# Kernel optimization log

Measured on AMD Instinct MI355X. Metric: run time of the kernel, lower is better.

Reference implementation:

```python
import jax, jax.numpy as jnp
import numpy as np

TEMP = 0.07
BASE_TEMP = 0.07
LOSS_WEIGHT = 0.5
BN_EPS = 1e-5


def _embed(x, w1, b1, gamma, beta, w2, b2):
    # 1x1 conv C->C  (x: [N,C,H,W], w1: [C_out,C_in])
    h = jnp.einsum('nchw,oc->nohw', x, w1) + b1[None, :, None, None]
    # BatchNorm2d in training mode: batch stats over (N,H,W), biased variance
    mean = h.mean(axis=(0, 2, 3), keepdims=True)
    var = h.var(axis=(0, 2, 3), keepdims=True)
    h = (h - mean) * jax.lax.rsqrt(var + BN_EPS)
    h = h * gamma[None, :, None, None] + beta[None, :, None, None]
    h = jax.nn.relu(h)
    h = jnp.einsum('nchw,oc->nohw', h, w2) + b2[None, :, None, None]
    # F.normalize(p=2, dim=1) with eps=1e-12
    nrm = jnp.sqrt(jnp.sum(h * h, axis=1, keepdims=True))
    return h / jnp.maximum(nrm, 1e-12)


def _contrastive(feats_, labels_):
    # feats_: [T, n_view, C]; labels_: [T]
    T, n_view, C = feats_.shape
    mask_small = (labels_[:, None] == labels_[None, :]).astype(feats_.dtype)  # [T,T]
    # torch.cat(torch.unbind(feats_, dim=1), dim=0): view-major ordering
    cf = feats_.transpose(1, 0, 2).reshape(T * n_view, C)
    logits = (cf @ cf.T) / TEMP                                   # [M,M], M=T*n_view
    logits = logits - jax.lax.stop_gradient(jnp.max(logits, axis=1, keepdims=True))
    mask = jnp.tile(mask_small, (n_view, n_view))                  # repeat(anchor_count, contrast_count)
    neg_mask = 1.0 - mask                                          # computed BEFORE diagonal removal
    M = T * n_view
    logits_mask = 1.0 - jnp.eye(M, dtype=feats_.dtype)
    mask = mask * logits_mask
    exp_logits = jnp.exp(logits)
    neg_logits = jnp.sum(exp_logits * neg_mask, axis=1, keepdims=True)
    log_prob = logits - jnp.log(exp_logits + neg_logits)
    mean_log_prob_pos = jnp.sum(mask * log_prob, axis=1) / (jnp.sum(mask, axis=1) + 1e-6)
    loss = -(TEMP / BASE_TEMP) * mean_log_prob_pos
    return jnp.mean(loss)


def setup_inputs() -> dict:
    N, C_in, H, W = 8, 512, 128, 128
    feat_dim, num_classes = 256, 19
    max_views, max_samples, ignore_label = 100, 1024, -1
    rng = np.random.RandomState(0)

    preds_S = rng.randn(N, C_in, H, W).astype(np.float32)
    # gt label map already at (H,W) => nearest interpolation is identity
    gt = rng.randint(0, num_classes, (N, H * W))
    logits_S = rng.randn(N, num_classes, H * W).astype(np.float32)
    predict = logits_S.argmax(axis=1)  # [N, H*W]

    # ---- replicate _hard_anchor_sampling on host (fixed seed) ----
    classes, total = [], 0
    for i in range(N):
        cl = [int(c) for c in np.unique(gt[i])
              if c != ignore_label and (gt[i] == c).sum() > max_views]
        classes.append(cl)
        total += len(cl)
    n_view = min(max_samples // total, max_views)

    b_idx, p_idx, y_cls = [], [], []
    for i in range(N):
        for c in classes[i]:
            hard = np.where((predict[i] == c) & (gt[i] != c))[0]
            easy = np.where((predict[i] == c) & (gt[i] == c))[0]
            nh, ne = len(hard), len(easy)
            if nh >= n_view / 2 and ne >= n_view / 2:
                kh = n_view // 2; ke = n_view - kh
            elif nh >= n_view / 2:
                ke = ne; kh = n_view - ke
            else:
                kh = nh; ke = n_view - kh
            hs = hard[rng.permutation(nh)[:kh]]
            es = easy[rng.permutation(ne)[:ke]]
            b_idx.append(i)
            p_idx.append(np.concatenate([hs, es]))
            y_cls.append(c)

    batch_idx = jnp.asarray(np.array(b_idx), dtype=jnp.int32)          # [T]
    pix_idx = jnp.asarray(np.stack(p_idx), dtype=jnp.int32)            # [T, n_view]
    y_cls = jnp.asarray(np.array(y_cls), dtype=jnp.int32)              # [T]

    def p(shape, scale, k):
        r = np.random.RandomState(k)
        return jnp.asarray((r.randn(*shape) * scale).astype(np.float32))

    return {
        'preds_S': jnp.asarray(preds_S),
        'w1': p((C_in, C_in), 0.02, 1),
        'b1': jnp.zeros((C_in,), jnp.float32),
        'gamma': jnp.ones((C_in,), jnp.float32),
        'beta': jnp.zeros((C_in,), jnp.float32),
        'w2': p((feat_dim, C_in), 0.02, 2),
        'b2': jnp.zeros((feat_dim,), jnp.float32),
        'batch_idx': batch_idx,
        'pix_idx': pix_idx,
        'y_cls': y_cls,
    }


def reference(preds_S, w1, b1, gamma, beta, w2, b2, batch_idx, pix_idx, y_cls):
    f = _embed(preds_S, w1, b1, gamma, beta, w2, b2)        # [N, C, H, W]
    N, C, H, W = f.shape
    feats = f.transpose(0, 2, 3, 1).reshape(N, H * W, C)     # [N, HW, C]
    X_ = feats[batch_idx[:, None], pix_idx]                   # [T, n_view, C]
    labels_ = y_cls.astype(f.dtype)
    return LOSS_WEIGHT * _contrastive(X_, labels_)
```

## Files before the change

kernel.cpp:

```cpp
#include <hip/hip_runtime.h>
#include <hip/hip_bf16.h>

#define C_IN   512
#define C_OUT  256
#define HW     16384
#define NIMG   8
#define PTOT   (NIMG * HW)
#define MP     1024
#define TEMP_INV (1.0f / 0.07f)
#define BN_EPS   1e-5f
#define SPB    4
#define OGRP   8
#define IGRP   8
#define BK     64

typedef float  f32x4  __attribute__((ext_vector_type(4)));
typedef short  short8 __attribute__((ext_vector_type(8)));
typedef short  short4v __attribute__((ext_vector_type(4)));

#define WS_S1   0
#define WS_G    (WS_S1 + C_IN)
#define WS_W1P  (WS_G + C_IN * C_IN)
#define WS_B1P  (WS_W1P + C_IN * C_IN)
#define WS_CF   (WS_B1P + C_IN)
#define WS_XB_F (WS_CF + MP * C_OUT)
#define WS_NEED_FAST ((size_t)WS_XB_F * 4 + (size_t)PTOT * C_IN * 2)

__global__ __launch_bounds__(256)
void kprep(const float* __restrict__ x, __hip_bfloat16* __restrict__ xb,
           float* __restrict__ s1) {
    int plane = blockIdx.x;
    int c = plane & (C_IN - 1);
    const float4* p = (const float4*)(x + (size_t)plane * HW);
    short4v* q = (short4v*)(xb + (size_t)plane * HW);
    float acc = 0.f;
    for (int i = threadIdx.x; i < HW / 4; i += 256) {
        float4 v = p[i];
        acc += v.x + v.y + v.z + v.w;
        union { short4v s; __hip_bfloat162 h[2]; } u;
        u.h[0] = __float22bfloat162_rn(make_float2(v.x, v.y));
        u.h[1] = __float22bfloat162_rn(make_float2(v.z, v.w));
        q[i] = u.s;
    }
    for (int off = 32; off; off >>= 1) acc += __shfl_down(acc, off, 64);
    __shared__ float red[4];
    int lane = threadIdx.x & 63, wv = threadIdx.x >> 6;
    if (lane == 0) red[wv] = acc;
    __syncthreads();
    if (threadIdx.x == 0)
        atomicAdd(&s1[c], red[0] + red[1] + red[2] + red[3]);
}

__global__ __launch_bounds__(256)
void ksum(const float* __restrict__ x, float* __restrict__ s1) {
    int plane = blockIdx.x;
    int c = plane & (C_IN - 1);
    const float4* p = (const float4*)(x + (size_t)plane * HW);
    float acc = 0.f;
    for (int i = threadIdx.x; i < HW / 4; i += 256) {
        float4 v = p[i];
        acc += v.x + v.y + v.z + v.w;
    }
    for (int off = 32; off; off >>= 1) acc += __shfl_down(acc, off, 64);
    __shared__ float red[4];
    int lane = threadIdx.x & 63, wv = threadIdx.x >> 6;
    if (lane == 0) red[wv] = acc;
    __syncthreads();
    if (threadIdx.x == 0)
        atomicAdd(&s1[c], red[0] + red[1] + red[2] + red[3]);
}

__device__ const int TILE_I[10] = {0,0,0,0,1,1,1,2,2,3};
__device__ const int TILE_J[10] = {0,1,2,3,1,2,3,2,3,3};

__global__ __launch_bounds__(256, 4)
void kgram_bf16(const __hip_bfloat16* __restrict__ xb, float* __restrict__ G) {
    __shared__ __hip_bfloat16 Abuf[128 * BK];
    __shared__ __hip_bfloat16 Bbuf[128 * BK];
    int tile  = blockIdx.x;
    int chunk = blockIdx.y;
    int n   = chunk >> 4;
    int hw0 = (chunk & 15) * 1024;
    int wave = threadIdx.x >> 6;
    int lane = threadIdx.x & 63;
    int wi = wave >> 1, wj = wave & 1;
    int IT = TILE_I[tile] * 128;
    int JT = TILE_J[tile] * 128;

    const __hip_bfloat16* gA = xb + ((size_t)n * C_IN + IT) * HW + hw0;
    const __hip_bfloat16* gB = xb + ((size_t)n * C_IN + JT) * HW + hw0;

    int rrel = lane >> 3;
    int slot = lane & 7;

    f32x4 acc[4][4];
#pragma unroll
    for (int i = 0; i < 4; ++i)
#pragma unroll
        for (int j = 0; j < 4; ++j) acc[i][j] = {0.f, 0.f, 0.f, 0.f};

    int m  = lane & 15;
    int kq = lane >> 4;

#pragma unroll 1
    for (int s = 0; s < 16; ++s) {
        int kk = s * BK;
#pragma unroll
        for (int i_ = 0; i_ < 4; ++i_) {
            int row = wave * 32 + i_ * 8 + rrel;
            int g   = slot ^ (row & 7);
            __builtin_amdgcn_global_load_lds(
                (const __attribute__((address_space(1))) void*)
                    (gA + (size_t)row * HW + kk + g * 8),
                (__attribute__((address_space(3))) void*)
                    (&Abuf[(wave * 32 + i_ * 8) * BK]),
                16, 0, 0);
            __builtin_amdgcn_global_load_lds(
                (const __attribute__((address_space(1))) void*)
                    (gB + (size_t)row * HW + kk + g * 8),
                (__attribute__((address_space(3))) void*)
                    (&Bbuf[(wave * 32 + i_ * 8) * BK]),
                16, 0, 0);
        }
        __syncthreads();
#pragma unroll
        for (int h = 0; h < 2; ++h) {
            short8 af[4], bf[4];
#pragma unroll
            for (int t = 0; t < 4; ++t) {
                int ra = wi * 64 + t * 16 + m;
                int qa = (h * 4 + kq) ^ (ra & 7);
                af[t] = *(const short8*)&Abuf[ra * BK + qa * 8];
                int rb = wj * 64 + t * 16 + m;
                int qb = (h * 4 + kq) ^ (rb & 7);
                bf[t] = *(const short8*)&Bbuf[rb * BK + qb * 8];
            }
#pragma unroll
            for (int i_ = 0; i_ < 4; ++i_)
#pragma unroll
                for (int j_ = 0; j_ < 4; ++j_)
                    acc[i_][j_] = __builtin_amdgcn_mfma_f32_16x16x32_bf16(
                        af[i_], bf[j_], acc[i_][j_], 0, 0, 0);
        }
        __syncthreads();
    }

    int r0 = (lane >> 4) * 4;
    int cc = lane & 15;
#pragma unroll
    for (int i = 0; i < 4; ++i)
#pragma unroll
        for (int j = 0; j < 4; ++j)
#pragma unroll
            for (int r = 0; r < 4; ++r)
                atomicAdd(&G[(size_t)(IT + wi * 64 + i * 16 + r0 + r) * C_IN
                             + (JT + wj * 64 + j * 16 + cc)],
                          acc[i][j][r]);
}

__global__ __launch_bounds__(256)
void kmirror(float* __restrict__ G) {
    int i = blockIdx.x;
    for (int j = threadIdx.x; j < C_IN; j += 256) {
        if ((i >> 7) > (j >> 7))
            G[(size_t)i * C_IN + j] = G[(size_t)j * C_IN + i];
    }
}

__device__ inline short8 load_frag_f32(const float* p) {
    float4 a = *(const float4*)p;
    float4 b = *(const float4*)(p + 4);
    union { short8 s; __hip_bfloat162 h[4]; } u;
    u.h[0] = __float22bfloat162_rn(make_float2(a.x, a.y));
    u.h[1] = __float22bfloat162_rn(make_float2(a.z, a.w));
    u.h[2] = __float22bfloat162_rn(make_float2(b.x, b.y));
    u.h[3] = __float22bfloat162_rn(make_float2(b.z, b.w));
    return u.s;
}

__global__ __launch_bounds__(256)
void kgram_f32(const float* __restrict__ x, float* __restrict__ G) {
    int bz  = blockIdx.z;
    int n   = bz >> 2;
    int hw0 = (bz & 3) * 4096;
    int wave = threadIdx.x >> 6;
    int lane = threadIdx.x & 63;
    int wi = wave >> 1, wj = wave & 1;
    int I0 = blockIdx.x * 128 + wi * 64;
    int J0 = blockIdx.y * 128 + wj * 64;
    int m    = lane & 15;
    int koff = (lane >> 4) * 8;

    const float* baseA[4];
    const float* baseB[4];
#pragma unroll
    for (int t = 0; t < 4; ++t) {
        baseA[t] = x + ((size_t)n * C_IN + (I0 + t * 16 + m)) * HW + hw0 + koff;
        baseB[t] = x + ((size_t)n * C_IN + (J0 + t * 16 + m)) * HW + hw0 + koff;
    }

    f32x4 acc[4][4];
#pragma unroll
    for (int i = 0; i < 4; ++i)
#pragma unroll
        for (int j = 0; j < 4; ++j) acc[i][j] = {0.f, 0.f, 0.f, 0.f};

    for (int kk = 0; kk < 4096; kk += 32) {
        short8 afr[4], bfr[4];
#pragma unroll
        for (int t = 0; t < 4; ++t) {
            afr[t] = load_frag_f32(baseA[t] + kk);
            bfr[t] = load_frag_f32(baseB[t] + kk);
        }
#pragma unroll
        for (int i = 0; i < 4; ++i)
#pragma unroll
            for (int j = 0; j < 4; ++j)
                acc[i][j] = __builtin_amdgcn_mfma_f32_16x16x32_bf16(
                    afr[i], bfr[j], acc[i][j], 0, 0, 0);
    }

    int r0 = (lane >> 4) * 4;
    int cc = lane & 15;
#pragma unroll
    for (int i = 0; i < 4; ++i)
#pragma unroll
        for (int j = 0; j < 4; ++j)
#pragma unroll
            for (int r = 0; r < 4; ++r)
                atomicAdd(&G[(size_t)(I0 + i * 16 + r0 + r) * C_IN + (J0 + j * 16 + cc)],
                          acc[i][j][r]);
}

__global__ __launch_bounds__(256)
void kstats(const float* __restrict__ w1, const float* __restrict__ b1,
            const float* __restrict__ gamma, const float* __restrict__ beta,
            const float* __restrict__ s1, const float* __restrict__ G,
            float* __restrict__ w1p, float* __restrict__ b1p) {
    int o0 = blockIdx.x * OGRP;
    int tid = threadIdx.x;
    __shared__ float wr[OGRP][C_IN];
    __shared__ float redd[4][OGRP];
    __shared__ float redq[4][OGRP];
    __shared__ float alpha_s[OGRP];

    for (int idx = tid; idx < OGRP * C_IN; idx += 256) {
        int og = idx >> 9, c = idx & (C_IN - 1);
        wr[og][c] = w1[(size_t)(o0 + og) * C_IN + c];
    }
    __syncthreads();

    float dot1[OGRP], quad[OGRP];
#pragma unroll
    for (int og = 0; og < OGRP; ++og) { dot1[og] = 0.f; quad[og] = 0.f; }

    for (int c = tid; c < C_IN; c += 256) {
        const float* gr = G + (size_t)c * C_IN;
        float s1c = s1[c];
        float inner[OGRP];
#pragma unroll
        for (int og = 0; og < OGRP; ++og) inner[og] = 0.f;
        for (int d = 0; d < C_IN; d += 4) {
            float4 gv = *(const float4*)(gr + d);
#pragma unroll
            for (int og = 0; og < OGRP; ++og) {
                float4 wv = *(const float4*)(&wr[og][d]);
                inner[og] += gv.x * wv.x + gv.y * wv.y + gv.z * wv.z + gv.w * wv.w;
            }
        }
#pragma unroll
        for (int og = 0; og < OGRP; ++og) {
            float wc = wr[og][c];
            quad[og] += inner[og] * wc;
            dot1[og] += s1c * wc;
        }
    }
#pragma unroll
    for (int og = 0; og < OGRP; ++og) {
        for (int off = 32; off; off >>= 1) {
            dot1[og] += __shfl_down(dot1[og], off, 64);
            quad[og] += __shfl_down(quad[og], off, 64);
        }
    }
    int lane = tid & 63, wv = tid >> 6;
    if (lane == 0) {
#pragma unroll
        for (int og = 0; og < OGRP; ++og) { redd[wv][og] = dot1[og]; redq[wv][og] = quad[og]; }
    }
    __syncthreads();
    if (tid < OGRP) {
        int og = tid;
        float d1 = redd[0][og] + redd[1][og] + redd[2][og] + redd[3][og];
        float q  = redq[0][og] + redq[1][og] + redq[2][og] + redq[3][og];
        float b  = b1[o0 + og];
        float mean = d1 / (float)PTOT + b;
        float eh2  = (q + 2.f * b * d1) / (float)PTOT + b * b;
        float var  = eh2 - mean * mean;
        float al   = gamma[o0 + og] * rsqrtf(var + BN_EPS);
        alpha_s[og] = al;
        b1p[o0 + og] = beta[o0 + og] + al * (b - mean);
    }
    __syncthreads();
    for (int idx = tid; idx < OGRP * C_IN; idx += 256) {
        int og = idx >> 9, c = idx & (C_IN - 1);
        w1p[(size_t)(o0 + og) * C_IN + c] = alpha_s[og] * wr[og][c];
    }
}

__global__ __launch_bounds__(256)
void kfeat(const float* __restrict__ x, const float* __restrict__ w1p,
           const float* __restrict__ b1p, const float* __restrict__ w2,
           const float* __restrict__ b2, const int* __restrict__ batch_idx,
           const int* __restrict__ pix_idx, float* __restrict__ cf,
           int M, int T, int n_view) {
    __shared__ float xcol[SPB][C_IN];
    __shared__ float h1[SPB][C_IN];
    __shared__ float fl[SPB][C_OUT];
    int tid = threadIdx.x;
    int m0 = blockIdx.x * SPB;

    for (int idx = tid; idx < SPB * C_IN; idx += 256) {
        int s = idx >> 9, c = idx & (C_IN - 1);
        int mm = m0 + s;
        float v = 0.f;
        if (mm < M) {
            int t = mm % T, vv = mm / T;
            int n = batch_idx[t];
            int pix = pix_idx[t * n_view + vv];
            v = x[((size_t)n * C_IN + c) * HW + pix];
        }
        xcol[s][c] = v;
    }
    __syncthreads();

    for (int o = tid; o < C_IN; o += 256) {
        float acc[SPB];
        float bb = b1p[o];
#pragma unroll
        for (int s = 0; s < SPB; ++s) acc[s] = bb;
        const float* wrp = w1p + (size_t)o * C_IN;
        for (int c = 0; c < C_IN; c += 4) {
            float4 w = *(const float4*)(wrp + c);
#pragma unroll
            for (int s = 0; s < SPB; ++s) {
                float4 xv = *(const float4*)(&xcol[s][c]);
                acc[s] += w.x * xv.x + w.y * xv.y + w.z * xv.z + w.w * xv.w;
            }
        }
#pragma unroll
        for (int s = 0; s < SPB; ++s) h1[s][o] = fmaxf(acc[s], 0.f);
    }
    __syncthreads();

    {
        int j = tid;
        float acc[SPB];
        float bb = b2[j];
#pragma unroll
        for (int s = 0; s < SPB; ++s) acc[s] = bb;
        const float* wrp = w2 + (size_t)j * C_IN;
        for (int o = 0; o < C_IN; o += 4) {
            float4 w = *(const float4*)(wrp + o);
#pragma unroll
            for (int s = 0; s < SPB; ++s) {
                float4 hv = *(const float4*)(&h1[s][o]);
                acc[s] += w.x * hv.x + w.y * hv.y + w.z * hv.z + w.w * hv.w;
            }
        }
#pragma unroll
        for (int s = 0; s < SPB; ++s) fl[s][j] = acc[s];
    }
    __syncthreads();

    int wv = tid >> 6, lane = tid & 63;
    {
        float sq = 0.f;
#pragma unroll
        for (int k = 0; k < 4; ++k) { float v = fl[wv][lane + 64 * k]; sq += v * v; }
        for (int off = 32; off; off >>= 1) sq += __shfl_down(sq, off, 64);
        float nrm = __shfl(sq, 0, 64);
        float rinv = 1.f / fmaxf(sqrtf(nrm), 1e-12f);
        int mm = m0 + wv;
        if (mm < M) {
#pragma unroll
            for (int k = 0; k < 4; ++k)
                cf[(size_t)mm * C_OUT + lane + 64 * k] = fl[wv][lane + 64 * k] * rinv;
        }
    }
}

__global__ __launch_bounds__(256)
void kloss(const float* __restrict__ cf, const int* __restrict__ y_cls,
           float* __restrict__ out, int M, int T) {
    int i0 = blockIdx.x * IGRP;
    int tid = threadIdx.x;
    __shared__ float ci[IGRP][C_OUT];
    __shared__ float row[IGRP][MP];
    __shared__ int   lbl[MP];
    __shared__ float redl[IGRP];
    int lane = tid & 63, wv = tid >> 6;

    for (int idx = tid; idx < IGRP * C_OUT; idx += 256) {
        int g = idx >> 8, c = idx & (C_OUT - 1);
        int ii = i0 + g;
        ci[g][c] = (ii < M) ? cf[(size_t)ii * C_OUT + c] : 0.f;
    }
    for (int j = tid; j < M; j += 256) lbl[j] = y_cls[j % T];
    __syncthreads();

    for (int j = tid; j < M; j += 256) {
        const float* cj = cf + (size_t)j * C_OUT;
        float acc[IGRP];
#pragma unroll
        for (int g = 0; g < IGRP; ++g) acc[g] = 0.f;
        for (int c = 0; c < C_OUT; c += 4) {
            float4 v = *(const float4*)(cj + c);
#pragma unroll
            for (int g = 0; g < IGRP; ++g) {
                float4 cv = *(const float4*)(&ci[g][c]);
                acc[g] += cv.x * v.x + cv.y * v.y + cv.z * v.z + cv.w * v.w;
            }
        }
#pragma unroll
        for (int g = 0; g < IGRP; ++g) row[g][j] = acc[g] * TEMP_INV;
    }
    __syncthreads();

    for (int g = wv; g < IGRP; g += 4) {
        int i = i0 + g;
        if (i < M) {
            int lbl_i = lbl[i];
            const float* r = row[g];

            float mx = -1e30f;
            for (int j = lane; j < M; j += 64) mx = fmaxf(mx, r[j]);
            for (int off = 32; off; off >>= 1) mx = fmaxf(mx, __shfl_down(mx, off, 64));
            mx = __shfl(mx, 0, 64);

            float neg = 0.f;
            for (int j = lane; j < M; j += 64)
                if (lbl[j] != lbl_i) neg += expf(r[j] - mx);
            for (int off = 32; off; off >>= 1) neg += __shfl_down(neg, off, 64);
            neg = __shfl(neg, 0, 64);

            float pos = 0.f; int cnt = 0;
            for (int j = lane; j < M; j += 64) {
                if (lbl[j] == lbl_i && j != i) {
                    float l = r[j] - mx;
                    pos += l - logf(expf(l) + neg);
                    cnt++;
                }
            }
            for (int off = 32; off; off >>= 1) {
                pos += __shfl_down(pos, off, 64);
                cnt += __shfl_down(cnt, off, 64);
            }
            if (lane == 0) redl[g] = -pos / ((float)cnt + 1e-6f);
        } else if (lane == 0) redl[g] = 0.f;
    }
    __syncthreads();
    if (tid == 0) {
        float s = 0.f;
        for (int g = 0; g < IGRP; ++g) s += redl[g];
        atomicAdd(out, s * (0.5f / (float)M));
    }
}

extern "C" void kernel_launch(void* const* d_in, const int* in_sizes, int n_in,
                              void* d_out, int out_size, void* d_ws, size_t ws_size,
                              hipStream_t stream) {
    const float* x     = (const float*)d_in[0];
    const float* w1    = (const float*)d_in[1];
    const float* b1    = (const float*)d_in[2];
    const float* gamma = (const float*)d_in[3];
    const float* beta  = (const float*)d_in[4];
    const float* w2    = (const float*)d_in[5];
    const float* b2    = (const float*)d_in[6];
    const int* batch_idx = (const int*)d_in[7];
    const int* pix_idx   = (const int*)d_in[8];
    const int* y_cls     = (const int*)d_in[9];

    int T = in_sizes[7];
    int M = in_sizes[8];
    int n_view = M / T;

    float* ws  = (float*)d_ws;
    float* s1  = ws + WS_S1;
    float* G   = ws + WS_G;
    float* w1p = ws + WS_W1P;
    float* b1p = ws + WS_B1P;
    float* cf  = ws + WS_CF;
    __hip_bfloat16* xb = (__hip_bfloat16*)(ws + WS_XB_F);

    hipMemsetAsync(s1, 0, (size_t)(C_IN + C_IN * C_IN) * sizeof(float), stream);
    hipMemsetAsync(d_out, 0, sizeof(float), stream);

    if (ws_size >= WS_NEED_FAST) {
        kprep<<<NIMG * C_IN, 256, 0, stream>>>(x, xb, s1);
        kgram_bf16<<<dim3(10, 128), 256, 0, stream>>>(xb, G);
        kmirror<<<C_IN, 256, 0, stream>>>(G);
    } else {
        ksum<<<NIMG * C_IN, 256, 0, stream>>>(x, s1);
        kgram_f32<<<dim3(4, 4, 32), 256, 0, stream>>>(x, G);
    }
    kstats<<<C_IN / OGRP, 256, 0, stream>>>(w1, b1, gamma, beta, s1, G, w1p, b1p);
    kfeat<<<(M + SPB - 1) / SPB, 256, 0, stream>>>(x, w1p, b1p, w2, b2,
                                                   batch_idx, pix_idx, cf, M, T, n_view);
    kloss<<<(M + IGRP - 1) / IGRP, 256, 0, stream>>>(cf, y_cls, (float*)d_out, M, T);
}
```

Measured before the change: 699.2 us.

## Replace Gram atomics with partial-tile buffers and reduction kernel; split diagonal tiles

The Gram-matrix kernel is split into diagonal and off-diagonal variants, so diagonal tiles load a single LDS buffer and reuse it for both operands. When enough workspace exists, each chunk writes its 128x128 partial tile to a scratch buffer instead of issuing float atomics, and a new reduction kernel sums the 128 partials, writing each tile and its mirror. This removes atomic contention and the separate mirror kernel and memset of G, at the cost of an extra ~84 MB write and read of partials. OGRP and IGRP are also halved, changing the block granularity of the stats and loss kernels.

New measurement: 672.5 us. -3.8%, faster.

```diff
diff --git a/kernel.cpp b/kernel.cpp
--- a/kernel.cpp
+++ b/kernel.cpp
@@ -10,8 +10,8 @@
 #define TEMP_INV (1.0f / 0.07f)
 #define BN_EPS   1e-5f
 #define SPB    4
-#define OGRP   8
-#define IGRP   8
+#define OGRP   4
+#define IGRP   4
 #define BK     64
 
 typedef float  f32x4  __attribute__((ext_vector_type(4)));
@@ -25,6 +25,9 @@
 #define WS_CF   (WS_B1P + C_IN)
 #define WS_XB_F (WS_CF + MP * C_OUT)
 #define WS_NEED_FAST ((size_t)WS_XB_F * 4 + (size_t)PTOT * C_IN * 2)
+#define WS_PART_F (WS_XB_F + PTOT * (C_IN / 2))
+#define NPART_F   (10 * 128 * 128 * 128)
+#define WS_NEED_PART ((size_t)(WS_PART_F + NPART_F) * 4)
 
 __global__ __launch_bounds__(256)
 void kprep(const float* __restrict__ x, __hip_bfloat16* __restrict__ xb,
@@ -70,22 +73,27 @@
         atomicAdd(&s1[c], red[0] + red[1] + red[2] + red[3]);
 }
 
-__device__ const int TILE_I[10] = {0,0,0,0,1,1,1,2,2,3};
-__device__ const int TILE_J[10] = {0,1,2,3,1,2,3,2,3,3};
-
+__device__ const int OI[6] = {0,0,0,1,1,2};
+__device__ const int OJ[6] = {1,2,3,2,3,3};
+__device__ const int TI2[10] = {0,1,2,3, 0,0,0,1,1,2};
+__device__ const int TJ2[10] = {0,1,2,3, 1,2,3,2,3,3};
+
+template<bool PART, bool DIAG>
 __global__ __launch_bounds__(256, 4)
-void kgram_bf16(const __hip_bfloat16* __restrict__ xb, float* __restrict__ G) {
+void kgram2(const __hip_bfloat16* __restrict__ xb, float* __restrict__ G,
+            float* __restrict__ Gp) {
     __shared__ __hip_bfloat16 Abuf[128 * BK];
-    __shared__ __hip_bfloat16 Bbuf[128 * BK];
-    int tile  = blockIdx.x;
+    __shared__ __hip_bfloat16 Bsto[DIAG ? 64 : 128 * BK];
+    int t     = blockIdx.x;
     int chunk = blockIdx.y;
     int n   = chunk >> 4;
     int hw0 = (chunk & 15) * 1024;
     int wave = threadIdx.x >> 6;
     int lane = threadIdx.x & 63;
     int wi = wave >> 1, wj = wave & 1;
-    int IT = TILE_I[tile] * 128;
-    int JT = TILE_J[tile] * 128;
+    int IT, JT;
+    if (DIAG) { IT = t * 128; JT = IT; }
+    else      { IT = OI[t] * 128; JT = OJ[t] * 128; }
 
     const __hip_bfloat16* gA = xb + ((size_t)n * C_IN + IT) * HW + hw0;
     const __hip_bfloat16* gB = xb + ((size_t)n * C_IN + JT) * HW + hw0;
@@ -115,25 +123,27 @@
                 (__attribute__((address_space(3))) void*)
                     (&Abuf[(wave * 32 + i_ * 8) * BK]),
                 16, 0, 0);
-            __builtin_amdgcn_global_load_lds(
-                (const __attribute__((address_space(1))) void*)
-                    (gB + (size_t)row * HW + kk + g * 8),
-                (__attribute__((address_space(3))) void*)
-                    (&Bbuf[(wave * 32 + i_ * 8) * BK]),
-                16, 0, 0);
+            if (!DIAG)
+                __builtin_amdgcn_global_load_lds(
+                    (const __attribute__((address_space(1))) void*)
+                        (gB + (size_t)row * HW + kk + g * 8),
+                    (__attribute__((address_space(3))) void*)
+                        (&Bsto[(wave * 32 + i_ * 8) * BK]),
+                    16, 0, 0);
         }
         __syncthreads();
 #pragma unroll
         for (int h = 0; h < 2; ++h) {
             short8 af[4], bf[4];
 #pragma unroll
-            for (int t = 0; t < 4; ++t) {
-                int ra = wi * 64 + t * 16 + m;
+            for (int t_ = 0; t_ < 4; ++t_) {
+                int ra = wi * 64 + t_ * 16 + m;
                 int qa = (h * 4 + kq) ^ (ra & 7);
-                af[t] = *(const short8*)&Abuf[ra * BK + qa * 8];
-                int rb = wj * 64 + t * 16 + m;
+                af[t_] = *(const short8*)&Abuf[ra * BK + qa * 8];
+                int rb = wj * 64 + t_ * 16 + m;
                 int qb = (h * 4 + kq) ^ (rb & 7);
-                bf[t] = *(const short8*)&Bbuf[rb * BK + qb * 8];
+                bf[t_] = DIAG ? *(const short8*)&Abuf[rb * BK + qb * 8]
+                              : *(const short8*)&Bsto[rb * BK + qb * 8];
             }
 #pragma unroll
             for (int i_ = 0; i_ < 4; ++i_)
@@ -147,15 +157,52 @@
 
     int r0 = (lane >> 4) * 4;
     int cc = lane & 15;
-#pragma unroll
-    for (int i = 0; i < 4; ++i)
-#pragma unroll
-        for (int j = 0; j < 4; ++j)
-#pragma unroll
-            for (int r = 0; r < 4; ++r)
-                atomicAdd(&G[(size_t)(IT + wi * 64 + i * 16 + r0 + r) * C_IN
-                             + (JT + wj * 64 + j * 16 + cc)],
-                          acc[i][j][r]);
+    if (PART) {
+        int tileid = DIAG ? t : (4 + t);
+        float* P = Gp + ((size_t)tileid * 128 + chunk) * (128 * 128);
+#pragma unroll
+        for (int i = 0; i < 4; ++i)
+#pragma unroll
+            for (int j = 0; j < 4; ++j)
+#pragma unroll
+                for (int r = 0; r < 4; ++r)
+                    P[(wi * 64 + i * 16 + r0 + r) * 128 + (wj * 64 + j * 16 + cc)]
+                        = acc[i][j][r];
+    } else {
+#pragma unroll
+        for (int i = 0; i < 4; ++i)
+#pragma unroll
+            for (int j = 0; j < 4; ++j)
+#pragma unroll
+                for (int r = 0; r < 4; ++r)
+                    atomicAdd(&G[(size_t)(IT + wi * 64 + i * 16 + r0 + r) * C_IN
+                                 + (JT + wj * 64 + j * 16 + cc)],
+                              acc[i][j][r]);
+    }
+}
+
+__global__ __launch_bounds__(256)
+void kgacc(const float* __restrict__ Gp, float* __restrict__ G) {
+    int tile = blockIdx.x >> 4;
+    int seg  = blockIdx.x & 15;
+    int IT = TI2[tile] * 128, JT = TJ2[tile] * 128;
+    int e0 = seg * 1024 + threadIdx.x * 4;
+    const float* base = Gp + (size_t)tile * 128 * (128 * 128) + e0;
+    f32x4 a0 = {0,0,0,0}, a1 = {0,0,0,0}, a2 = {0,0,0,0}, a3 = {0,0,0,0};
+    for (int ch = 0; ch < 128; ch += 4) {
+        a0 += *(const f32x4*)(base + (size_t)(ch + 0) * (128 * 128));
+        a1 += *(const f32x4*)(base + (size_t)(ch + 1) * (128 * 128));
+        a2 += *(const f32x4*)(base + (size_t)(ch + 2) * (128 * 128));
+        a3 += *(const f32x4*)(base + (size_t)(ch + 3) * (128 * 128));
+    }
+    f32x4 s = (a0 + a1) + (a2 + a3);
+    int r = e0 >> 7, c = e0 & 127;
+    *(f32x4*)(&G[(size_t)(IT + r) * C_IN + JT + c]) = s;
+    if (IT != JT) {
+#pragma unroll
+        for (int k = 0; k < 4; ++k)
+            G[(size_t)(JT + c + k) * C_IN + IT + r] = s[k];
+    }
 }
 
 __global__ __launch_bounds__(256)
@@ -491,15 +538,24 @@
     float* b1p = ws + WS_B1P;
     float* cf  = ws + WS_CF;
     __hip_bfloat16* xb = (__hip_bfloat16*)(ws + WS_XB_F);
-
-    hipMemsetAsync(s1, 0, (size_t)(C_IN + C_IN * C_IN) * sizeof(float), stream);
+    float* Gpart = ws + WS_PART_F;
+
     hipMemsetAsync(d_out, 0, sizeof(float), stream);
 
-    if (ws_size >= WS_NEED_FAST) {
+    if (ws_size >= WS_NEED_PART) {
+        hipMemsetAsync(s1, 0, (size_t)C_IN * sizeof(float), stream);
         kprep<<<NIMG * C_IN, 256, 0, stream>>>(x, xb, s1);
-        kgram_bf16<<<dim3(10, 128), 256, 0, stream>>>(xb, G);
+        kgram2<true, true ><<<dim3(4, 128), 256, 0, stream>>>(xb, G, Gpart);
+        kgram2<true, false><<<dim3(6, 128), 256, 0, stream>>>(xb, G, Gpart);
+        kgacc<<<160, 256, 0, stream>>>(Gpart, G);
+    } else if (ws_size >= WS_NEED_FAST) {
+        hipMemsetAsync(s1, 0, (size_t)(C_IN + C_IN * C_IN) * sizeof(float), stream);
+        kprep<<<NIMG * C_IN, 256, 0, stream>>>(x, xb, s1);
+        kgram2<false, true ><<<dim3(4, 128), 256, 0, stream>>>(xb, G, nullptr);
+        kgram2<false, false><<<dim3(6, 128), 256, 0, stream>>>(xb, G, nullptr);
         kmirror<<<C_IN, 256, 0, stream>>>(G);
     } else {
+        hipMemsetAsync(s1, 0, (size_t)(C_IN + C_IN * C_IN) * sizeof(float), stream);
         ksum<<<NIMG * C_IN, 256, 0, stream>>>(x, s1);
         kgram_f32<<<dim3(4, 4, 32), 256, 0, stream>>>(x, G);
     }
```
